# Kernel tuning notes

Measured on AMD Instinct MI355X. Metric: run time of the kernel, lower is better.

The kernel has to match this reference:

```python
import jax, jax.numpy as jnp
import numpy as np

N_HIDDEN = 8
N_CLASSES = 10
TIME_STEPS = 28
INPUT_DIM = 28
FORGET_BIAS = 1.0


def setup_inputs() -> dict:
    key = jax.random.key(0)
    k1, k2, k3, k4 = jax.random.split(key, 4)
    B = 32768
    x = jax.random.normal(k1, (B, TIME_STEPS, INPUT_DIM), dtype=jnp.float32)
    # BasicLSTMCell kernel: [input_dim + hidden, 4*hidden], gate order i, j, f, o
    W_lstm = jax.random.normal(k2, (INPUT_DIM + N_HIDDEN, 4 * N_HIDDEN), dtype=jnp.float32) * 0.1
    b_lstm = jnp.zeros((4 * N_HIDDEN,), dtype=jnp.float32)  # TF zero-init bias
    out_weights = jax.random.normal(k3, (N_HIDDEN, N_CLASSES), dtype=jnp.float32)
    out_biases = jax.random.normal(k4, (N_CLASSES,), dtype=jnp.float32)
    return {"x": x, "W_lstm": W_lstm, "b_lstm": b_lstm,
            "out_weights": out_weights, "out_biases": out_biases}


def reference(x, W_lstm, b_lstm, out_weights, out_biases):
    B = x.shape[0]

    def step(carry, xt):
        c, h = carry
        gates = jnp.concatenate([xt, h], axis=-1) @ W_lstm + b_lstm  # [B, 4H]
        i, j, f, o = jnp.split(gates, 4, axis=-1)  # BasicLSTMCell order: i, j, f, o
        new_c = c * jax.nn.sigmoid(f + FORGET_BIAS) + jax.nn.sigmoid(i) * jnp.tanh(j)
        new_h = jnp.tanh(new_c) * jax.nn.sigmoid(o)
        return (new_c, new_h), None

    xs = jnp.swapaxes(x, 0, 1)  # [T, B, input_dim]
    init = (jnp.zeros((B, N_HIDDEN), x.dtype), jnp.zeros((B, N_HIDDEN), x.dtype))
    (_, last_h), _ = jax.lax.scan(step, init, xs)
    logits = last_h @ out_weights + out_biases  # [B, n_classes]
    return logits
```

## Files before the change

kernel.cpp:

```cpp
#include <hip/hip_runtime.h>


#define TSTEPS 28
#define DIN    28
#define NH     8
#define NG     32
#define NC     10
#define NROWS  36

__device__ __forceinline__ float fast_exp2(float x) {
    return __builtin_amdgcn_exp2f(x);
}
__device__ __forceinline__ float fast_rcp(float x) {
    return __builtin_amdgcn_rcpf(x);
}
__device__ __forceinline__ float fast_sigmoid(float z) {
    return fast_rcp(1.0f + fast_exp2(-1.4426950408889634f * z));
}
__device__ __forceinline__ float fast_tanh(float z) {
    return 1.0f - 2.0f * fast_rcp(1.0f + fast_exp2(2.8853900817779268f * z));
}

__global__ __launch_bounds__(256, 2) void lstm_kernel(
    const float* __restrict__ x,
    const float* __restrict__ W,
    const float* __restrict__ bias,
    const float* __restrict__ Wout,
    const float* __restrict__ bout,
    float* __restrict__ out)
{
    const int tid  = blockIdx.x * 256 + threadIdx.x;
    const int e    = tid >> 3;
    const int u    = tid & 7;
    const int lane = threadIdx.x & 63;
    const int base8 = lane & ~7;

    const float* xb = x + (size_t)e * (TSTEPS * DIN);

    float Wr[NROWS][4];
#pragma unroll
    for (int k = 0; k < NROWS; ++k) {
#pragma unroll
        for (int gt = 0; gt < 4; ++gt)
            Wr[k][gt] = W[k * NG + gt * NH + u];
    }
    float bg[4];
#pragma unroll
    for (int gt = 0; gt < 4; ++gt) bg[gt] = bias[gt * NH + u];

    float c = 0.0f;
    float hall[NH];
#pragma unroll
    for (int j = 0; j < NH; ++j) hall[j] = 0.0f;

    float4 xq[7];
    {
        const float4* xv = (const float4*)xb;
#pragma unroll
        for (int i = 0; i < 7; ++i) xq[i] = xv[i];
    }

#pragma unroll 1
    for (int t = 0; t < TSTEPS; ++t) {
        float xt[DIN];
#pragma unroll
        for (int i = 0; i < 7; ++i) {
            xt[4*i+0] = xq[i].x; xt[4*i+1] = xq[i].y;
            xt[4*i+2] = xq[i].z; xt[4*i+3] = xq[i].w;
        }
        if (t + 1 < TSTEPS) {
            const float4* xv = (const float4*)(xb + (t + 1) * DIN);
#pragma unroll
            for (int i = 0; i < 7; ++i) xq[i] = xv[i];
        }

        float g[4];
#pragma unroll
        for (int gt = 0; gt < 4; ++gt) g[gt] = bg[gt];

#pragma unroll
        for (int k = 0; k < DIN; ++k) {
#pragma unroll
            for (int gt = 0; gt < 4; ++gt)
                g[gt] = fmaf(xt[k], Wr[k][gt], g[gt]);
        }
#pragma unroll
        for (int k = 0; k < NH; ++k) {
#pragma unroll
            for (int gt = 0; gt < 4; ++gt)
                g[gt] = fmaf(hall[k], Wr[DIN + k][gt], g[gt]);
        }

        float ig = fast_sigmoid(g[0]);
        float jg = fast_tanh(g[1]);
        float fg = fast_sigmoid(g[2] + 1.0f);
        float og = fast_sigmoid(g[3]);
        c = c * fg + ig * jg;
        float hu = fast_tanh(c) * og;

#pragma unroll
        for (int j = 0; j < NH; ++j)
            hall[j] = __shfl(hu, base8 + j, 64);
    }

    float acc = bout[u];
#pragma unroll
    for (int k = 0; k < NH; ++k)
        acc = fmaf(hall[k], Wout[k * NC + u], acc);
    out[(size_t)e * NC + u] = acc;

    if (u < 2) {
        float acc1 = bout[NH + u];
#pragma unroll
        for (int k = 0; k < NH; ++k)
            acc1 = fmaf(hall[k], Wout[k * NC + NH + u], acc1);
        out[(size_t)e * NC + NH + u] = acc1;
    }
}

extern "C" void kernel_launch(void* const* d_in, const int* in_sizes, int n_in,
                              void* d_out, int out_size, void* d_ws, size_t ws_size,
                              hipStream_t stream) {
    const float* x    = (const float*)d_in[0];
    const float* W    = (const float*)d_in[1];
    const float* b    = (const float*)d_in[2];
    const float* Wout = (const float*)d_in[3];
    const float* bout = (const float*)d_in[4];
    float* out = (float*)d_out;

    const int B = in_sizes[0] / (TSTEPS * DIN);
    const int threads = B * NH;
    const int block = 256;
    const int grid = threads / block;
    lstm_kernel<<<grid, block, 0, stream>>>(x, W, b, Wout, bout, out);
}
```

Measured before the change: 176.9 us.

## Assign one thread per LSTM gate column and exchange gates via ds_swizzle

The kernel now maps 32 threads to each batch element, one per gate column, instead of 8 threads each computing all four gates. Each thread computes a single activation, selected per lane with constants so the sigmoid and tanh paths share one formula. The i/j/f/o values and the hidden state are exchanged with ds_swizzle instead of __shfl. This shortens the per-thread dependency chain, cuts register use and raises occupancy (launch bounds go to 4 blocks). In exchange, x loads are repeated by 4x more threads and the cell update and tanh(c) are computed redundantly across gate groups.

```diff
diff --git a/kernel.cpp b/kernel.cpp
--- a/kernel.cpp
+++ b/kernel.cpp
@@ -8,20 +8,13 @@
 #define NC     10
 #define NROWS  36
 
-__device__ __forceinline__ float fast_exp2(float x) {
-    return __builtin_amdgcn_exp2f(x);
-}
-__device__ __forceinline__ float fast_rcp(float x) {
-    return __builtin_amdgcn_rcpf(x);
-}
-__device__ __forceinline__ float fast_sigmoid(float z) {
-    return fast_rcp(1.0f + fast_exp2(-1.4426950408889634f * z));
-}
-__device__ __forceinline__ float fast_tanh(float z) {
-    return 1.0f - 2.0f * fast_rcp(1.0f + fast_exp2(2.8853900817779268f * z));
-}
+__device__ __forceinline__ float fexp2(float x) { return __builtin_amdgcn_exp2f(x); }
+__device__ __forceinline__ float frcp(float x)  { return __builtin_amdgcn_rcpf(x); }
 
-__global__ __launch_bounds__(256, 2) void lstm_kernel(
+#define SWZ(v, imm) \
+    __int_as_float(__builtin_amdgcn_ds_swizzle(__float_as_int(v), (imm)))
+
+__global__ __launch_bounds__(256, 4) void lstm_kernel(
     const float* __restrict__ x,
     const float* __restrict__ W,
     const float* __restrict__ bias,
@@ -29,24 +22,21 @@
     const float* __restrict__ bout,
     float* __restrict__ out)
 {
-    const int tid  = blockIdx.x * 256 + threadIdx.x;
-    const int e    = tid >> 3;
-    const int u    = tid & 7;
-    const int lane = threadIdx.x & 63;
-    const int base8 = lane & ~7;
+    const int tid = blockIdx.x * 256 + threadIdx.x;
+    const int e   = tid >> 5;
+    const int l5  = threadIdx.x & 31;
+    const int gt  = l5 >> 3;
 
     const float* xb = x + (size_t)e * (TSTEPS * DIN);
 
-    float Wr[NROWS][4];
+    float Wr[NROWS];
 #pragma unroll
-    for (int k = 0; k < NROWS; ++k) {
-#pragma unroll
-        for (int gt = 0; gt < 4; ++gt)
-            Wr[k][gt] = W[k * NG + gt * NH + u];
-    }
-    float bg[4];
-#pragma unroll
-    for (int gt = 0; gt < 4; ++gt) bg[gt] = bias[gt * NH + u];
+    for (int k = 0; k < NROWS; ++k) Wr[k] = W[k * NG + l5];
+
+    const float bg = bias[l5] + (gt == 2 ? 1.0f : 0.0f);
+    const float sK = (gt == 1) ?  2.8853900817779268f : -1.4426950408889634f;
+    const float mK = (gt == 1) ? -2.0f : 1.0f;
+    const float qK = (gt == 1) ?  1.0f : 0.0f;
 
     float c = 0.0f;
     float hall[NH];
@@ -74,47 +64,41 @@
             for (int i = 0; i < 7; ++i) xq[i] = xv[i];
         }
 
-        float g[4];
+        float g = bg;
 #pragma unroll
-        for (int gt = 0; gt < 4; ++gt) g[gt] = bg[gt];
+        for (int k = 0; k < DIN; ++k)
+            g = fmaf(xt[k], Wr[k], g);
+#pragma unroll
+        for (int k = 0; k < NH; ++k)
+            g = fmaf(hall[k], Wr[DIN + k], g);
 
-#pragma unroll
-        for (int k = 0; k < DIN; ++k) {
-#pragma unroll
-            for (int gt = 0; gt < 4; ++gt)
-                g[gt] = fmaf(xt[k], Wr[k][gt], g[gt]);
-        }
-#pragma unroll
-        for (int k = 0; k < NH; ++k) {
-#pragma unroll
-            for (int gt = 0; gt < 4; ++gt)
-                g[gt] = fmaf(hall[k], Wr[DIN + k][gt], g[gt]);
-        }
+        float a = fmaf(mK, frcp(1.0f + fexp2(sK * g)), qK);
 
-        float ig = fast_sigmoid(g[0]);
-        float jg = fast_tanh(g[1]);
-        float fg = fast_sigmoid(g[2] + 1.0f);
-        float og = fast_sigmoid(g[3]);
-        c = c * fg + ig * jg;
-        float hu = fast_tanh(c) * og;
+        float iv = SWZ(a, 0x0007);
+        float jv = SWZ(a, 0x0107);
+        float fv = SWZ(a, 0x0207);
+        float ov = SWZ(a, 0x0307);
 
-#pragma unroll
-        for (int j = 0; j < NH; ++j)
-            hall[j] = __shfl(hu, base8 + j, 64);
+        c = fmaf(c, fv, iv * jv);
+        float th = fmaf(-2.0f, frcp(1.0f + fexp2(2.8853900817779268f * c)), 1.0f);
+        float hu = th * ov;
+
+        hall[0] = SWZ(hu, 0x0000);
+        hall[1] = SWZ(hu, 0x0020);
+        hall[2] = SWZ(hu, 0x0040);
+        hall[3] = SWZ(hu, 0x0060);
+        hall[4] = SWZ(hu, 0x0080);
+        hall[5] = SWZ(hu, 0x00A0);
+        hall[6] = SWZ(hu, 0x00C0);
+        hall[7] = SWZ(hu, 0x00E0);
     }
 
-    float acc = bout[u];
-#pragma unroll
-    for (int k = 0; k < NH; ++k)
-        acc = fmaf(hall[k], Wout[k * NC + u], acc);
-    out[(size_t)e * NC + u] = acc;
-
-    if (u < 2) {
-        float acc1 = bout[NH + u];
+    if (l5 < NC) {
+        float acc = bout[l5];
 #pragma unroll
         for (int k = 0; k < NH; ++k)
-            acc1 = fmaf(hall[k], Wout[k * NC + NH + u], acc1);
-        out[(size_t)e * NC + NH + u] = acc1;
+            acc = fmaf(hall[k], Wout[k * NC + l5], acc);
+        out[(size_t)e * NC + l5] = acc;
     }
 }
 
@@ -129,7 +113,7 @@
     float* out = (float*)d_out;
 
     const int B = in_sizes[0] / (TSTEPS * DIN);
-    const int threads = B * NH;
+    const int threads = B * NG;
     const int block = 256;
     const int grid = threads / block;
     lstm_kernel<<<grid, block, 0, stream>>>(x, W, b, Wout, bout, out);
```

After: 256.6 us. 1.45x slower.
